# Kernel tuning notes

Hardware: AMD Instinct MI355X
Metric: run time of the kernel (lower is better)

## Reference

```python
import jax, jax.numpy as jnp
import numpy as np

N = 50000      # nodes
E = 800000     # edges (before self loops)
F_IN = 16      # n_input_features
PRE = 32       # n_channels_preproc
C = 128        # n_channels
GH = 32        # edge_gate_hidden_dim
L = 5          # n_gnn_layers (tied weights)


def setup_inputs() -> dict:
    key = jax.random.key(0)
    ks = jax.random.split(key, 16)
    def w(k, shape):
        return jax.random.normal(k, shape, jnp.float32) * 0.05
    return dict(
        x=jax.random.normal(ks[0], (N, F_IN), jnp.float32),
        edge_index=jax.random.randint(ks[1], (2, E), 0, N),
        edge_attr=jax.random.normal(ks[2], (E, 1), jnp.float32),
        W_pre=w(ks[3], (F_IN, PRE)), b_pre=jnp.zeros((PRE,), jnp.float32),
        W_init=w(ks[4], (PRE, C)), b_init=jnp.zeros((C,), jnp.float32),
        W_g1=w(ks[5], (2 * C + 1, GH)), b_g1=jnp.zeros((GH,), jnp.float32),
        W_g2=w(ks[6], (GH, 1)), b_g2=jnp.zeros((1,), jnp.float32),
        W_z=w(ks[7], (2 * C, C)), b_z=jnp.zeros((C,), jnp.float32),
        W_r=w(ks[8], (2 * C, C)), b_r=jnp.zeros((C,), jnp.float32),
        W_h=w(ks[9], (2 * C, C)), b_h=jnp.zeros((C,), jnp.float32),
        W_f1=w(ks[10], (2 * C, C)), b_f1=jnp.zeros((C,), jnp.float32),
        W_f2=w(ks[11], (C, 2)), b_f2=jnp.zeros((2,), jnp.float32),
    )


def reference(x, edge_index, edge_attr,
              W_pre, b_pre, W_init, b_init,
              W_g1, b_g1, W_g2, b_g2,
              W_z, b_z, W_r, b_r, W_h, b_h,
              W_f1, b_f1, W_f2, b_f2):
    n = x.shape[0]
    # add self loops (fill_value=0.0 for edge_attr)
    sl = jnp.arange(n)
    row = jnp.concatenate([edge_index[0], sl])   # source (x_j)
    col = jnp.concatenate([edge_index[1], sl])   # target (x_i), aggregation index
    ea = jnp.concatenate([edge_attr, jnp.zeros((n, 1), x.dtype)], axis=0)
    # symmetric normalization from in-degree (degree of col, incl. self loops)
    deg = jax.ops.segment_sum(jnp.ones(col.shape[0], x.dtype), col, num_segments=n)
    dis = jnp.where(deg > 0, deg ** -0.5, 0.0)
    norm = (dis[row] * dis[col])[:, None]        # [E', 1]

    # preproc + initial node transform
    h = jax.nn.relu(x @ W_pre + b_pre)
    h0 = jax.nn.relu(h @ W_init + b_init)
    h = h0

    for _ in range(L):  # tied GGNN layers
        x_i = h[col]                              # gather target feats  [E', C]
        x_j = h[row]                              # gather source feats  [E', C]
        g_in = jnp.concatenate([x_i, x_j, ea], axis=-1)          # [E', 2C+1]
        gate = jax.nn.sigmoid(jax.nn.relu(g_in @ W_g1 + b_g1) @ W_g2 + b_g2)
        msg = gate * (norm * x_j)                                  # [E', C]
        aggr = jax.ops.segment_sum(msg, col, num_segments=n)       # scatter-add
        # GRU-style update
        za = jnp.concatenate([h, aggr], axis=-1)                   # [N, 2C]
        z = jax.nn.sigmoid(za @ W_z + b_z)
        r = jax.nn.sigmoid(za @ W_r + b_r)
        hc = jax.nn.relu(jnp.concatenate([r * h, aggr], axis=-1) @ W_h + b_h)
        h = (1.0 - z) * h + z * hc

    out = jnp.concatenate([h0, h], axis=-1)       # [N, 2C]
    out = jax.nn.relu(out @ W_f1 + b_f1)
    return out @ W_f2 + b_f2                      # [N, 2] logits (output_activation='none')
```

## Files before the change

kernel.cpp:

```cpp
#include <hip/hip_runtime.h>
#include <math.h>

#define NODES 50000
#define NEDGES 800000
#define ETOT (NEDGES + NODES)
#define FIN 16
#define PRE 32
#define C 128
#define GH 32
#define LAYERS 5
#define RECS 160
#define SCB 64
#define SCT 256
#define SCCH ((NODES + SCB*SCT - 1) / (SCB*SCT))
#define NB ((NODES + 255) >> 8)
#define BCAP 6144
#define LOUTC (BCAP + 256)
#define BIN_BLOCKS 98
#define EPB ((NEDGES + BIN_BLOCKS - 1) / BIN_BLOCKS)

typedef _Float16 f16;
typedef f16 f16x8 __attribute__((ext_vector_type(8)));
typedef f16 f16x4 __attribute__((ext_vector_type(4)));
typedef f16 f16x2 __attribute__((ext_vector_type(2)));
typedef float f32x4 __attribute__((ext_vector_type(4)));

__device__ __forceinline__ float sigmoidf_(float x) { return 1.0f / (1.0f + __expf(-x)); }

__device__ __forceinline__ int swz_off(int row, int bytecol, int stride) {
    return row * stride + ((((bytecol) >> 4) ^ (row & 7)) << 4) + (bytecol & 15);
}
__device__ __forceinline__ int ps_off(int row, int bytecol) {
    return row * 64 + ((((bytecol) >> 4) ^ (row & 3)) << 4) + (bytecol & 15);
}

__device__ __forceinline__ int bperm(int c) { return 4 * (c & 7) + (c >> 3); }

__global__ void k_degree(const int* __restrict__ col, float* __restrict__ deg) {
    int e = blockIdx.x * blockDim.x + threadIdx.x;
    if (e < NEDGES) atomicAdd(&deg[col[e]], 1.0f);
}

__global__ __launch_bounds__(SCT) void k_scan1(const float* __restrict__ deg, int* __restrict__ bsum) {
    __shared__ int ws4[SCT / 64];
    int b = blockIdx.x, t = threadIdx.x;
    int lane = t & 63, wv = t >> 6;
    int base = (b * SCT + t) * SCCH;
    int sum = 0;
#pragma unroll
    for (int j = 0; j < SCCH; j++) {
        int i = base + j;
        if (i < NODES) sum += (int)deg[i] + 1;
    }
#pragma unroll
    for (int off = 32; off > 0; off >>= 1) sum += __shfl_xor(sum, off, 64);
    if (lane == 0) ws4[wv] = sum;
    __syncthreads();
    if (t == 0) {
        int tot = 0;
#pragma unroll
        for (int j = 0; j < SCT / 64; j++) tot += ws4[j];
        bsum[b] = tot;
    }
}

__global__ __launch_bounds__(64) void k_scan2(const int* __restrict__ bsum, int* __restrict__ bscan,
                                              int* __restrict__ start) {
    int t = threadIdx.x;
    int v = (t < SCB) ? bsum[t] : 0;
    int x = v;
#pragma unroll
    for (int off = 1; off < 64; off <<= 1) {
        int tt = __shfl_up(x, off, 64);
        if (t >= off) x += tt;
    }
    if (t < SCB) bscan[t] = x - v;
    if (t == SCB - 1) start[NODES] = x;
}

__global__ __launch_bounds__(SCT) void k_scan3(
    float* __restrict__ deg_dis, float* __restrict__ rdis, const int* __restrict__ bscan,
    int* __restrict__ start) {
    __shared__ int woff[SCT / 64];
    int b = blockIdx.x, t = threadIdx.x;
    int lane = t & 63, wv = t >> 6;
    int base = (b * SCT + t) * SCCH;
    int v[SCCH]; int sum = 0;
#pragma unroll
    for (int j = 0; j < SCCH; j++) {
        int i = base + j;
        v[j] = (i < NODES) ? (int)deg_dis[i] + 1 : 0;
        sum += v[j];
    }
    int x = sum;
#pragma unroll
    for (int off = 1; off < 64; off <<= 1) {
        int tt = __shfl_up(x, off, 64);
        if (lane >= off) x += tt;
    }
    int texcl = x - sum;
    if (lane == 63) woff[wv] = x;
    __syncthreads();
    int wbase = 0;
    for (int j = 0; j < wv; j++) wbase += woff[j];
    int run = bscan[b] + wbase + texcl;
#pragma unroll
    for (int j = 0; j < SCCH; j++) {
        int i = base + j;
        if (i < NODES) {
            start[i] = run;
            float fv = (float)v[j];
            deg_dis[i] = rsqrtf(fv);
            rdis[i] = sqrtf(fv);
        }
        run += v[j];
    }
}

__global__ __launch_bounds__(256) void k_bucket2(
    const int* __restrict__ eidx, const float* __restrict__ eattr,
    int* __restrict__ bcnt , int2* __restrict__ bbuf) {
    __shared__ int cnt[NB];
    __shared__ int gbase[NB];
    __shared__ int cur[NB];
    int b = blockIdx.x, t = threadIdx.x;
    int e0 = b * EPB;
    int e1 = e0 + EPB; if (e1 > NEDGES) e1 = NEDGES;
    for (int i = t; i < NB; i += 256) cnt[i] = 0;
    __syncthreads();
    for (int e = e0 + t; e < e1; e += 256) {
        int ci = eidx[NEDGES + e];
        atomicAdd(&cnt[ci >> 8], 1);
    }
    __syncthreads();
    for (int i = t; i < NB; i += 256) {
        gbase[i] = (cnt[i] > 0) ? atomicAdd(&bcnt[i * 16], cnt[i]) : 0;
        cur[i] = 0;
    }
    __syncthreads();
    for (int e = e0 + t; e < e1; e += 256) {
        int r = eidx[e], ci = eidx[NEDGES + e];
        float ea = eattr[e];
        int bk = ci >> 8;
        int pos = gbase[bk] + atomicAdd(&cur[bk], 1);
        if (pos < BCAP)
            bbuf[(size_t)bk * BCAP + pos] =
                make_int2((r & 0xFFFF) | ((ci & 255) << 16), __float_as_int(ea));
    }
}

__global__ __launch_bounds__(256) void k_csr2(
    const int* __restrict__ bcnt, const int2* __restrict__ bbuf,
    const int* __restrict__ start, int2* __restrict__ esort) {
    __shared__ int2 lout[LOUTC];
    __shared__ int lcur[256];
    int b = blockIdx.x, t = threadIdx.x;
    int lo = b << 8;
    int hi = lo + 256; if (hi > NODES) hi = NODES;
    int nn = hi - lo;
    int sbase = start[lo];
    int total = start[hi] - sbase;
    if (t < nn) lcur[t] = start[lo + t] - sbase;
    __syncthreads();
    int n = bcnt[b * 16]; if (n > BCAP) n = BCAP;
    for (int i = t; i < n; i += 256) {
        int2 w = bbuf[(size_t)b * BCAP + i];
        int cil = (w.x >> 16) & 255;
        int r = w.x & 0xFFFF;
        int pos = atomicAdd(&lcur[cil], 1);
        if (pos < LOUTC) lout[pos] = make_int2(r, w.y);
    }
    if (t < nn) {
        int pos = atomicAdd(&lcur[t], 1);
        if (pos < LOUTC) lout[pos] = make_int2(lo + t, 0);
    }
    __syncthreads();
    int lim = total < LOUTC ? total : LOUTC;
    for (int i = t; i < lim; i += 256) esort[sbase + i] = lout[i];
}

__global__ __launch_bounds__(256) void k_prep_w(
    const float* __restrict__ Wz, const float* __restrict__ Wr, const float* __restrict__ Wh,
    const float* __restrict__ Wg1, const float* __restrict__ Wf1,
    const float* __restrict__ Wpre, const float* __restrict__ Winit,
    f16* __restrict__ WcatF, f16* __restrict__ WhtopF, f16* __restrict__ Wg1F,
    f16* __restrict__ Wf1F, f16* __restrict__ WpreF, f16* __restrict__ WinitF) {
    int t = blockIdx.x * 256 + threadIdx.x;
    int l = t & 63;
    int lr = l & 15, lh = l >> 4;
    if (t < 24 * 8 * 64) {
        int idx = t >> 6; int nt = idx >> 3, ks = idx & 7;
        int wv = nt / 6, ntl = nt % 6;
        int grp = ntl >> 1, pr = ntl & 1;
        int ncol = (2 * wv + pr) * 16 + lr;
        f16x8 v;
#pragma unroll
        for (int j = 0; j < 8; j++) {
            int k = ks * 32 + lh * 8 + j;
            float x;
            if (grp == 0)      x = Wz[k * 128 + ncol];
            else if (grp == 1) x = Wr[k * 128 + ncol];
            else               x = (k >= 128) ? Wh[k * 128 + ncol] : 0.0f;
            v[j] = (f16)x;
        }
        *(f16x8*)(WcatF + (size_t)t * 8) = v;
    } else if (t < 24 * 8 * 64 + 8 * 4 * 64) {
        int t2 = t - 24 * 8 * 64;
        int idx = t2 >> 6; int nt = idx >> 2, ks = idx & 3;
        int n = nt * 16 + lr;
        f16x8 v;
#pragma unroll
        for (int j = 0; j < 8; j++) {
            int k = ks * 32 + lh * 8 + j;
            v[j] = (f16)Wh[k * 128 + n];
        }
        *(f16x8*)(WhtopF + (size_t)t2 * 8) = v;
    } else if (t < 24 * 8 * 64 + 8 * 4 * 64 + 4 * 4 * 64) {
        int t3 = t - (24 * 8 * 64 + 8 * 4 * 64);
        int idx = t3 >> 6; int nt = idx >> 2, ks = idx & 3;
        int cg = nt * 16 + lr;
        f16x8 v;
#pragma unroll
        for (int j = 0; j < 8; j++) {
            int k = ks * 32 + lh * 8 + j;
            v[j] = (f16)((cg < 32) ? Wg1[k * GH + cg] : Wg1[(128 + k) * GH + (cg - 32)]);
        }
        *(f16x8*)(Wg1F + (size_t)t3 * 8) = v;
    } else if (t < 24 * 8 * 64 + 8 * 4 * 64 + 4 * 4 * 64 + 8 * 8 * 64) {
        int t4 = t - (24 * 8 * 64 + 8 * 4 * 64 + 4 * 4 * 64);
        int idx = t4 >> 6; int nt = idx >> 3, ks = idx & 7;
        int n = nt * 16 + lr;
        f16x8 v;
#pragma unroll
        for (int j = 0; j < 8; j++) {
            int k = ks * 32 + lh * 8 + j;
            v[j] = (f16)Wf1[k * 128 + n];
        }
        *(f16x8*)(Wf1F + (size_t)t4 * 8) = v;
    } else if (t < 19456 + 2 * 64) {
        int t5 = t - 19456;
        int nt = t5 >> 6;
        f16x8 v;
#pragma unroll
        for (int j = 0; j < 8; j++) {
            int k = lh * 8 + j;
            v[j] = (k < FIN) ? (f16)Wpre[k * PRE + nt * 16 + lr] : (f16)0.0f;
        }
        *(f16x8*)(WpreF + (size_t)t5 * 8) = v;
    } else if (t < 19456 + 128 + 8 * 64) {
        int t6 = t - 19456 - 128;
        int nt = t6 >> 6;
        f16x8 v;
#pragma unroll
        for (int j = 0; j < 8; j++) {
            int k = lh * 8 + j;
            v[j] = (f16)Winit[k * C + nt * 16 + lr];
        }
        *(f16x8*)(WinitF + (size_t)t6 * 8) = v;
    }
}

__global__ __launch_bounds__(256) void k_pre_gate(
    const float* __restrict__ x, const float* __restrict__ bpre, const float* __restrict__ binit,
    const float* __restrict__ dis,
    const f16* __restrict__ WpreF, const f16* __restrict__ WinitF,
    const f16* __restrict__ Wg1F, const float* __restrict__ bg1,
    f16* __restrict__ h0_16, f16* __restrict__ rec,
    float* __restrict__ A) {
    __shared__ f16 ps[32 * 32];
    __shared__ f16 za[32 * 128];
    char* psB = (char*)ps;
    char* zaB = (char*)za;
    int tid = threadIdx.x;
    int l = tid & 63, w = tid >> 6;
    int lr = l & 15, lh = l >> 4;
    int n0 = blockIdx.x * 32;
    int rt0 = w >> 1, ct = w & 1;

    f16x8 xa = {};
    {
        int gn = n0 + rt0 * 16 + lr;
        if (gn < NODES && lh < 2) {
            float4 xv0 = *(const float4*)(x + (size_t)gn * FIN + lh * 8);
            float4 xv1 = *(const float4*)(x + (size_t)gn * FIN + lh * 8 + 4);
            xa[0] = (f16)xv0.x; xa[1] = (f16)xv0.y; xa[2] = (f16)xv0.z; xa[3] = (f16)xv0.w;
            xa[4] = (f16)xv1.x; xa[5] = (f16)xv1.y; xa[6] = (f16)xv1.z; xa[7] = (f16)xv1.w;
        }
    }
    f16x8 bA = *(const f16x8*)(WpreF + ((size_t)ct * 64 + l) * 8);
    f32x4 accA; accA[0] = accA[1] = accA[2] = accA[3] = 0.0f;
    accA = __builtin_amdgcn_mfma_f32_16x16x32_f16(xa, bA, accA, 0, 0, 0);
    {
        float bp = bpre[ct * 16 + lr];
#pragma unroll
        for (int j = 0; j < 4; j++) {
            int row = rt0 * 16 + lh * 4 + j;
            float v = fmaxf(accA[j] + bp, 0.0f);
            *(f16*)(psB + ps_off(row, (ct * 16 + lr) * 2)) = (f16)v;
        }
    }
    __syncthreads();

    f16x8 pa0 = *(const f16x8*)(psB + ps_off(lr, lh * 16));
    f16x8 pa1 = *(const f16x8*)(psB + ps_off(lr + 16, lh * 16));
    f32x4 accB[2][2];
#pragma unroll
    for (int rt = 0; rt < 2; rt++)
#pragma unroll
        for (int ntl = 0; ntl < 2; ntl++)
#pragma unroll
            for (int j = 0; j < 4; j++) accB[rt][ntl][j] = 0.0f;
#pragma unroll
    for (int ntl = 0; ntl < 2; ntl++) {
        f16x8 b = *(const f16x8*)(WinitF + ((size_t)((w * 2 + ntl) * 64 + l)) * 8);
        accB[0][ntl] = __builtin_amdgcn_mfma_f32_16x16x32_f16(pa0, b, accB[0][ntl], 0, 0, 0);
        accB[1][ntl] = __builtin_amdgcn_mfma_f32_16x16x32_f16(pa1, b, accB[1][ntl], 0, 0, 0);
    }
#pragma unroll
    for (int rt = 0; rt < 2; rt++)
#pragma unroll
        for (int ntl = 0; ntl < 2; ntl++) {
            int cg = (w * 2 + ntl) * 16 + lr;
            float bi = binit[cg];
#pragma unroll
            for (int j = 0; j < 4; j++) {
                int row = rt * 16 + lh * 4 + j;
                float v = fmaxf(accB[rt][ntl][j] + bi, 0.0f);
                *(f16*)(zaB + swz_off(row, cg * 2, 256)) = (f16)v;
            }
        }
    __syncthreads();

    for (int p = tid; p < 32 * 16; p += 256) {
        int row = p >> 4, seg = p & 15;
        int gn = n0 + row;
        if (gn < NODES) {
            f16x8 v = *(const f16x8*)(zaB + swz_off(row, seg * 16, 256));
            *(f16x8*)(h0_16 + (size_t)gn * C + seg * 8) = v;
            float dn = dis[gn];
            f16x8 od;
#pragma unroll
            for (int j = 0; j < 8; j++) od[j] = (f16)((float)v[j] * dn);
            *(f16x8*)(rec + (size_t)gn * RECS + 32 + seg * 8) = od;
        }
    }

    f32x4 acc3[2];
#pragma unroll
    for (int rt = 0; rt < 2; rt++)
#pragma unroll
        for (int j = 0; j < 4; j++) acc3[rt][j] = 0.0f;
#pragma unroll
    for (int ks = 0; ks < 4; ks++) {
        int kk = ks * 32 + lh * 8;
        f16x8 a0 = *(const f16x8*)(zaB + swz_off(lr,      kk * 2, 256));
        f16x8 a1 = *(const f16x8*)(zaB + swz_off(lr + 16, kk * 2, 256));
        f16x8 b = *(const f16x8*)(Wg1F + ((size_t)(w * 4 + ks) * 64 + l) * 8);
        acc3[0] = __builtin_amdgcn_mfma_f32_16x16x32_f16(a0, b, acc3[0], 0, 0, 0);
        acc3[1] = __builtin_amdgcn_mfma_f32_16x16x32_f16(a1, b, acc3[1], 0, 0, 0);
    }
    int col3 = w * 16 + lr;
#pragma unroll
    for (int rt = 0; rt < 2; rt++)
#pragma unroll
        for (int j = 0; j < 4; j++) {
            int row = rt * 16 + lh * 4 + j;
            int gn = n0 + row;
            if (gn < NODES) {
                float v = acc3[rt][j];
                if (col3 < 32) A[(size_t)gn * GH + bperm(col3)] = v + bg1[col3];
                else           rec[(size_t)gn * RECS + bperm(col3 - 32)] = (f16)v;
            }
        }
}

__global__ __launch_bounds__(256) void k_msg(
    const int* __restrict__ start, const int2* __restrict__ esort,
    const float* __restrict__ dis,
    const float* __restrict__ A, const f16* __restrict__ rec,
    const float* __restrict__ Wg1, const float* __restrict__ Wg2, const float* __restrict__ bg2,
    f16* __restrict__ aggr16) {
    int wid = (blockIdx.x * blockDim.x + threadIdx.x) >> 6;
    int lane = threadIdx.x & 63;
    if (wid >= NODES) return;
    int k8 = lane & 7;
    int q = lane >> 3;
    int s0 = start[wid], s1 = start[wid + 1];
    float4 a4 = *(const float4*)(A + (size_t)wid * GH + k8 * 4);
    const float* wg1e = Wg1 + 2 * C * GH;
    float wea0 = wg1e[k8], wea1 = wg1e[k8 + 8], wea2 = wg1e[k8 + 16], wea3 = wg1e[k8 + 24];
    float w20 = Wg2[k8], w21 = Wg2[k8 + 8], w22 = Wg2[k8 + 16], w23 = Wg2[k8 + 24];
    float b2 = bg2[0];
    float dci = dis[wid];
    float acc[16];
#pragma unroll
    for (int j = 0; j < 16; j++) acc[j] = 0.0f;

    int s = s0 + q;
    f16x8 ha0 = {}, hb0 = {};
    f16x4 bb0 = {};
    float ea0 = 0.0f;
    if (s < s1) {
        int2 e0 = esort[s];
        ea0 = __int_as_float(e0.y);
        const f16* rr = rec + (size_t)e0.x * RECS;
        bb0 = *(const f16x4*)(rr + k8 * 4);
        ha0 = *(const f16x8*)(rr + 32 + k8 * 16);
        hb0 = *(const f16x8*)(rr + 32 + k8 * 16 + 8);
    }
    while (s < s1) {
        int s2 = s + 8;
        f16x8 ha1 = {}, hb1 = {};
        f16x4 bb1 = {};
        float ea1 = 0.0f;
        if (s2 < s1) {
            int2 e1 = esort[s2];
            ea1 = __int_as_float(e1.y);
            const f16* rr = rec + (size_t)e1.x * RECS;
            bb1 = *(const f16x4*)(rr + k8 * 4);
            ha1 = *(const f16x8*)(rr + 32 + k8 * 16);
            hb1 = *(const f16x8*)(rr + 32 + k8 * 16 + 8);
        }
        float t0 = fmaxf(a4.x + (float)bb0[0] + ea0 * wea0, 0.0f);
        float t1 = fmaxf(a4.y + (float)bb0[1] + ea0 * wea1, 0.0f);
        float t2 = fmaxf(a4.z + (float)bb0[2] + ea0 * wea2, 0.0f);
        float t3 = fmaxf(a4.w + (float)bb0[3] + ea0 * wea3, 0.0f);
        float p = t0 * w20;
        p = fmaf(t1, w21, p);
        p = fmaf(t2, w22, p);
        p = fmaf(t3, w23, p);
        p += __shfl_xor(p, 4, 8);
        p += __shfl_xor(p, 2, 8);
        p += __shfl_xor(p, 1, 8);
        float coef = sigmoidf_(p + b2);
#pragma unroll
        for (int j = 0; j < 8; j++) {
            acc[j]     = fmaf(coef, (float)ha0[j], acc[j]);
            acc[8 + j] = fmaf(coef, (float)hb0[j], acc[8 + j]);
        }
        ha0 = ha1; hb0 = hb1; bb0 = bb1; ea0 = ea1;
        s = s2;
    }
#pragma unroll
    for (int j = 0; j < 16; j++) {
        acc[j] += __shfl_xor(acc[j], 8, 64);
        acc[j] += __shfl_xor(acc[j], 16, 64);
        acc[j] += __shfl_xor(acc[j], 32, 64);
    }
    if (lane < 8) {
        f16x8 o1, o2;
#pragma unroll
        for (int j = 0; j < 8; j++) { o1[j] = (f16)(acc[j] * dci); o2[j] = (f16)(acc[8 + j] * dci); }
        *(f16x8*)(aggr16 + (size_t)wid * C + k8 * 16) = o1;
        *(f16x8*)(aggr16 + (size_t)wid * C + k8 * 16 + 8) = o2;
    }
}

__global__ __launch_bounds__(256) void k_update_mfma(
    f16* __restrict__ rec, const f16* __restrict__ aggr16,
    const float* __restrict__ dis, const float* __restrict__ rdis,
    const f16* __restrict__ WcatF, const f16* __restrict__ WhtopF, const f16* __restrict__ Wg1F,
    const float* __restrict__ bz, const float* __restrict__ br, const float* __restrict__ bh,
    const float* __restrict__ bg1,
    float* __restrict__ A) {
    __shared__ f16 za[32 * 256];
    __shared__ f16 rhbuf[32 * 128];
    char* zaB = (char*)za;
    char* rhB = (char*)rhbuf;
    int tid = threadIdx.x;
    int l = tid & 63, w = tid >> 6;
    int lr = l & 15, lh = l >> 4;
    int n0 = blockIdx.x * 32;

    for (int p = tid; p < 32 * 16; p += 256) {
        int row = p >> 4, seg = p & 15;
        int gn = n0 + row;
        f16x8 v = {};
        if (gn < NODES) {
            v = *(const f16x8*)(rec + (size_t)gn * RECS + 32 + seg * 8);
            float rd = rdis[gn];
#pragma unroll
            for (int j = 0; j < 8; j++) v[j] = (f16)((float)v[j] * rd);
        }
        *(f16x8*)(zaB + swz_off(row, seg * 16, 512)) = v;
    }
    for (int p = tid; p < 32 * 16; p += 256) {
        int row = p >> 4, seg = p & 15;
        int gn = n0 + row;
        f16x8 v = {};
        if (gn < NODES) v = *(const f16x8*)(aggr16 + (size_t)gn * C + seg * 8);
        *(f16x8*)(zaB + swz_off(row, 256 + seg * 16, 512)) = v;
    }
    __syncthreads();

    f32x4 acc[2][6];
#pragma unroll
    for (int rt = 0; rt < 2; rt++)
#pragma unroll
        for (int n = 0; n < 6; n++)
#pragma unroll
            for (int j = 0; j < 4; j++) acc[rt][n][j] = 0.0f;
#pragma unroll
    for (int ks = 0; ks < 8; ks++) {
        int kk = ks * 32 + lh * 8;
        f16x8 a0 = *(const f16x8*)(zaB + swz_off(lr,      kk * 2, 512));
        f16x8 a1 = *(const f16x8*)(zaB + swz_off(lr + 16, kk * 2, 512));
#pragma unroll
        for (int ntl = 0; ntl < 6; ntl++) {
            f16x8 b = *(const f16x8*)(WcatF + ((size_t)((w * 6 + ntl) * 8 + ks) * 64 + l) * 8);
            acc[0][ntl] = __builtin_amdgcn_mfma_f32_16x16x32_f16(a0, b, acc[0][ntl], 0, 0, 0);
            acc[1][ntl] = __builtin_amdgcn_mfma_f32_16x16x32_f16(a1, b, acc[1][ntl], 0, 0, 0);
        }
    }

    float zreg[2][2][4];
#pragma unroll
    for (int rt = 0; rt < 2; rt++)
#pragma unroll
        for (int pr = 0; pr < 2; pr++) {
            int cg = (2 * w + pr) * 16 + lr;
#pragma unroll
            for (int j = 0; j < 4; j++) {
                int row = rt * 16 + lh * 4 + j;
                zreg[rt][pr][j] = sigmoidf_(acc[rt][pr][j] + bz[cg]);
                float rv = sigmoidf_(acc[rt][2 + pr][j] + br[cg]);
                float hv = (float)*(const f16*)(zaB + swz_off(row, cg * 2, 512));
                *(f16*)(rhB + swz_off(row, cg * 2, 256)) = (f16)(rv * hv);
            }
        }
    __syncthreads();

    f32x4 acc2[2][2];
#pragma unroll
    for (int rt = 0; rt < 2; rt++)
#pragma unroll
        for (int pr = 0; pr < 2; pr++) {
            int cg = (2 * w + pr) * 16 + lr;
#pragma unroll
            for (int j = 0; j < 4; j++)
                acc2[rt][pr][j] = acc[rt][4 + pr][j] + bh[cg];
        }
#pragma unroll
    for (int ks = 0; ks < 4; ks++) {
        int kk = ks * 32 + lh * 8;
        f16x8 a0 = *(const f16x8*)(rhB + swz_off(lr,      kk * 2, 256));
        f16x8 a1 = *(const f16x8*)(rhB + swz_off(lr + 16, kk * 2, 256));
#pragma unroll
        for (int pr = 0; pr < 2; pr++) {
            f16x8 b = *(const f16x8*)(WhtopF + ((size_t)((w * 2 + pr) * 4 + ks) * 64 + l) * 8);
            acc2[0][pr] = __builtin_amdgcn_mfma_f32_16x16x32_f16(a0, b, acc2[0][pr], 0, 0, 0);
            acc2[1][pr] = __builtin_amdgcn_mfma_f32_16x16x32_f16(a1, b, acc2[1][pr], 0, 0, 0);
        }
    }

#pragma unroll
    for (int rt = 0; rt < 2; rt++)
#pragma unroll
        for (int pr = 0; pr < 2; pr++) {
            int cg = (2 * w + pr) * 16 + lr;
#pragma unroll
            for (int j = 0; j < 4; j++) {
                int row = rt * 16 + lh * 4 + j;
                int gn = n0 + row;
                float hc = fmaxf(acc2[rt][pr][j], 0.0f);
                float z = zreg[rt][pr][j];
                float hold = (float)*(const f16*)(zaB + swz_off(row, cg * 2, 512));
                float hn = (1.0f - z) * hold + z * hc;
                if (gn < NODES) {
                    rec[(size_t)gn * RECS + 32 + cg] = (f16)(hn * dis[gn]);
                }
                *(f16*)(zaB + swz_off(row, cg * 2, 512)) = (f16)hn;
            }
        }
    __syncthreads();

    f32x4 acc3[2];
#pragma unroll
    for (int rt = 0; rt < 2; rt++)
#pragma unroll
        for (int j = 0; j < 4; j++) acc3[rt][j] = 0.0f;
#pragma unroll
    for (int ks = 0; ks < 4; ks++) {
        int kk = ks * 32 + lh * 8;
        f16x8 a0 = *(const f16x8*)(zaB + swz_off(lr,      kk * 2, 512));
        f16x8 a1 = *(const f16x8*)(zaB + swz_off(lr + 16, kk * 2, 512));
        f16x8 b = *(const f16x8*)(Wg1F + ((size_t)(w * 4 + ks) * 64 + l) * 8);
        acc3[0] = __builtin_amdgcn_mfma_f32_16x16x32_f16(a0, b, acc3[0], 0, 0, 0);
        acc3[1] = __builtin_amdgcn_mfma_f32_16x16x32_f16(a1, b, acc3[1], 0, 0, 0);
    }
    int col3 = w * 16 + lr;
#pragma unroll
    for (int rt = 0; rt < 2; rt++)
#pragma unroll
        for (int j = 0; j < 4; j++) {
            int row = rt * 16 + lh * 4 + j;
            int gn = n0 + row;
            if (gn < NODES) {
                float v = acc3[rt][j];
                if (col3 < 32) A[(size_t)gn * GH + bperm(col3)] = v + bg1[col3];
                else           rec[(size_t)gn * RECS + bperm(col3 - 32)] = (f16)v;
            }
        }
}

__global__ __launch_bounds__(256) void k_final_mfma(
    const f16* __restrict__ h0_16, const f16* __restrict__ rec, const float* __restrict__ rdis,
    const f16* __restrict__ Wf1F, const float* __restrict__ bf1,
    const float* __restrict__ Wf2, const float* __restrict__ bf2,
    float* __restrict__ out) {
    __shared__ float fs[32][132];
    char* zaB = (char*)&fs[0][0];
    int tid = threadIdx.x;
    int l = tid & 63, w = tid >> 6;
    int lr = l & 15, lh = l >> 4;
    int n0 = blockIdx.x * 32;

    for (int p = tid; p < 32 * 16; p += 256) {
        int row = p >> 4, seg = p & 15;
        int gn = n0 + row;
        f16x8 v = {};
        if (gn < NODES) v = *(const f16x8*)(h0_16 + (size_t)gn * C + seg * 8);
        *(f16x8*)(zaB + swz_off(row, seg * 16, 512)) = v;
    }
    for (int p = tid; p < 32 * 16; p += 256) {
        int row = p >> 4, seg = p & 15;
        int gn = n0 + row;
        f16x8 v = {};
        if (gn < NODES) {
            v = *(const f16x8*)(rec + (size_t)gn * RECS + 32 + seg * 8);
            float rd = rdis[gn];
#pragma unroll
            for (int j = 0; j < 8; j++) v[j] = (f16)((float)v[j] * rd);
        }
        *(f16x8*)(zaB + swz_off(row, 256 + seg * 16, 512)) = v;
    }
    __syncthreads();

    f32x4 acc[2][2];
#pragma unroll
    for (int rt = 0; rt < 2; rt++)
#pragma unroll
        for (int n = 0; n < 2; n++)
#pragma unroll
            for (int j = 0; j < 4; j++) acc[rt][n][j] = 0.0f;
#pragma unroll
    for (int ks = 0; ks < 8; ks++) {
        int kk = ks * 32 + lh * 8;
        f16x8 a0 = *(const f16x8*)(zaB + swz_off(lr,      kk * 2, 512));
        f16x8 a1 = *(const f16x8*)(zaB + swz_off(lr + 16, kk * 2, 512));
#pragma unroll
        for (int ntl = 0; ntl < 2; ntl++) {
            f16x8 b = *(const f16x8*)(Wf1F + ((size_t)((w * 2 + ntl) * 8 + ks) * 64 + l) * 8);
            acc[0][ntl] = __builtin_amdgcn_mfma_f32_16x16x32_f16(a0, b, acc[0][ntl], 0, 0, 0);
            acc[1][ntl] = __builtin_amdgcn_mfma_f32_16x16x32_f16(a1, b, acc[1][ntl], 0, 0, 0);
        }
    }
    __syncthreads();

#pragma unroll
    for (int rt = 0; rt < 2; rt++)
#pragma unroll
        for (int ntl = 0; ntl < 2; ntl++) {
            int cg = (w * 2 + ntl) * 16 + lr;
#pragma unroll
            for (int j = 0; j < 4; j++) {
                int row = rt * 16 + lh * 4 + j;
                fs[row][cg] = fmaxf(acc[rt][ntl][j] + bf1[cg], 0.0f);
            }
        }
    __syncthreads();

    if (tid < 64) {
        int n = tid >> 1, o = tid & 1;
        int gn = n0 + n;
        if (gn < NODES) {
            float a = bf2[o];
#pragma unroll 16
            for (int c = 0; c < C; c++) a = fmaf(fs[n][c], Wf2[c * 2 + o], a);
            out[(size_t)gn * 2 + o] = a;
        }
    }
}

extern "C" void kernel_launch(void* const* d_in, const int* in_sizes, int n_in,
                              void* d_out, int out_size, void* d_ws, size_t ws_size,
                              hipStream_t stream) {
    const float* x    = (const float*)d_in[0];
    const int*   eidx = (const int*)d_in[1];
    const float* eattr= (const float*)d_in[2];
    const float* Wpre = (const float*)d_in[3];  const float* bpre = (const float*)d_in[4];
    const float* Winit= (const float*)d_in[5];  const float* binit= (const float*)d_in[6];
    const float* Wg1  = (const float*)d_in[7];  const float* bg1  = (const float*)d_in[8];
    const float* Wg2  = (const float*)d_in[9];  const float* bg2  = (const float*)d_in[10];
    const float* Wz   = (const float*)d_in[11]; const float* bz   = (const float*)d_in[12];
    const float* Wr   = (const float*)d_in[13]; const float* br   = (const float*)d_in[14];
    const float* Wh   = (const float*)d_in[15]; const float* bh   = (const float*)d_in[16];
    const float* Wf1  = (const float*)d_in[17]; const float* bf1  = (const float*)d_in[18];
    const float* Wf2  = (const float*)d_in[19]; const float* bf2  = (const float*)d_in[20];
    float* out = (float*)d_out;

    float* ws  = (float*)d_ws;
    float* dis = ws;
    float* rdis= dis + NODES;
    float* A   = rdis + NODES;
    int*   start = (int*)(A + (size_t)NODES * GH);
    int*   bsum  = start + NODES + 1;
    int*   bscan = bsum + SCB;
    int*   bcnt  = bscan + SCB;
    int2*  bbuf  = (int2*)(((size_t)(bcnt + NB * 16) + 7) & ~(size_t)7);
    int2*  esort = bbuf + (size_t)NB * BCAP;
    size_t f16_base = (size_t)((int*)(esort + ETOT) - (int*)ws);
    f16_base = (f16_base + 3) & ~(size_t)3;
    f16* h0_16  = (f16*)(ws + f16_base);
    f16* rec    = h0_16 + (size_t)NODES * C;
    f16* aggr16 = rec + (size_t)NODES * RECS;
    f16* WcatF  = aggr16 + (size_t)NODES * C;
    f16* WhtopF = WcatF + 24 * 8 * 64 * 8;
    f16* Wg1F   = WhtopF + 8 * 4 * 64 * 8;
    f16* Wf1F   = Wg1F + 4 * 4 * 64 * 8;
    f16* WpreF  = Wf1F + 8 * 8 * 64 * 8;
    f16* WinitF = WpreF + 2 * 64 * 8;
    size_t f16_total = (size_t)NODES * (C + RECS + C)
                     + (24 * 8 + 8 * 4 + 4 * 4 + 8 * 8 + 2 + 8) * 64 * 8;
    const size_t REQ = (f16_base + (f16_total + 1) / 2) * sizeof(float);
    if (ws_size < REQ) return;

    hipMemsetAsync(dis, 0, NODES * sizeof(float), stream);
    hipMemsetAsync(bcnt, 0, NB * 16 * sizeof(int), stream);
    k_degree<<<(NEDGES + 255) / 256, 256, 0, stream>>>(eidx + NEDGES, dis);
    k_scan1<<<SCB, SCT, 0, stream>>>(dis, bsum);
    k_scan2<<<1, 64, 0, stream>>>(bsum, bscan, start);
    k_scan3<<<SCB, SCT, 0, stream>>>(dis, rdis, bscan, start);
    k_bucket2<<<BIN_BLOCKS, 256, 0, stream>>>(eidx, eattr, bcnt, bbuf);
    k_csr2<<<NB, 256, 0, stream>>>(bcnt, bbuf, start, esort);
    k_prep_w<<<(19456 + 128 + 512 + 255) / 256, 256, 0, stream>>>(
        Wz, Wr, Wh, Wg1, Wf1, Wpre, Winit, WcatF, WhtopF, Wg1F, Wf1F, WpreF, WinitF);
    k_pre_gate<<<(NODES + 31) / 32, 256, 0, stream>>>(
        x, bpre, binit, dis, WpreF, WinitF, Wg1F, bg1, h0_16, rec, A);

    for (int l = 0; l < LAYERS; l++) {
        k_msg<<<(NODES * 64 + 255) / 256, 256, 0, stream>>>(
            start, esort, dis, A, rec, Wg1, Wg2, bg2, aggr16);
        k_update_mfma<<<(NODES + 31) / 32, 256, 0, stream>>>(
            rec, aggr16, dis, rdis, WcatF, WhtopF, Wg1F, bz, br, bh, bg1, A);
    }
    k_final_mfma<<<(NODES + 31) / 32, 256, 0, stream>>>(h0_16, rec, rdis, Wf1F, bf1, Wf2, bf2, out);
}
```

Baseline: 557.8 us.

## Fuse message aggregation into GRU update kernel with ping-pong node buffers

Merges the per-node gated message aggregation kernel into the MFMA update kernel, so each block aggregates its 32 nodes directly into shared memory instead of writing and re-reading an f16 aggregate array. To avoid read/write races on node records across blocks, the record and gate-precompute arrays are double-buffered and swapped each layer. This removes one launch per layer and the aggr round trip. In exchange, each block of 256 threads now serialises 8 nodes per wave in the gather phase and may have lower occupancy, because the aggregation phase and the MFMA phase now live in one kernel that uses the shared-memory tiles.

```diff
diff --git a/kernel.cpp b/kernel.cpp
--- a/kernel.cpp
+++ b/kernel.cpp
@@ -374,95 +374,15 @@
         }
 }
 
-__global__ __launch_bounds__(256) void k_msg(
+__global__ __launch_bounds__(256) void k_layer(
     const int* __restrict__ start, const int2* __restrict__ esort,
-    const float* __restrict__ dis,
-    const float* __restrict__ A, const f16* __restrict__ rec,
+    const float* __restrict__ dis, const float* __restrict__ rdis,
+    const float* __restrict__ A_cur, const f16* __restrict__ recC,
+    f16* __restrict__ recN, float* __restrict__ A_nxt,
+    const f16* __restrict__ WcatF, const f16* __restrict__ WhtopF, const f16* __restrict__ Wg1F,
     const float* __restrict__ Wg1, const float* __restrict__ Wg2, const float* __restrict__ bg2,
-    f16* __restrict__ aggr16) {
-    int wid = (blockIdx.x * blockDim.x + threadIdx.x) >> 6;
-    int lane = threadIdx.x & 63;
-    if (wid >= NODES) return;
-    int k8 = lane & 7;
-    int q = lane >> 3;
-    int s0 = start[wid], s1 = start[wid + 1];
-    float4 a4 = *(const float4*)(A + (size_t)wid * GH + k8 * 4);
-    const float* wg1e = Wg1 + 2 * C * GH;
-    float wea0 = wg1e[k8], wea1 = wg1e[k8 + 8], wea2 = wg1e[k8 + 16], wea3 = wg1e[k8 + 24];
-    float w20 = Wg2[k8], w21 = Wg2[k8 + 8], w22 = Wg2[k8 + 16], w23 = Wg2[k8 + 24];
-    float b2 = bg2[0];
-    float dci = dis[wid];
-    float acc[16];
-#pragma unroll
-    for (int j = 0; j < 16; j++) acc[j] = 0.0f;
-
-    int s = s0 + q;
-    f16x8 ha0 = {}, hb0 = {};
-    f16x4 bb0 = {};
-    float ea0 = 0.0f;
-    if (s < s1) {
-        int2 e0 = esort[s];
-        ea0 = __int_as_float(e0.y);
-        const f16* rr = rec + (size_t)e0.x * RECS;
-        bb0 = *(const f16x4*)(rr + k8 * 4);
-        ha0 = *(const f16x8*)(rr + 32 + k8 * 16);
-        hb0 = *(const f16x8*)(rr + 32 + k8 * 16 + 8);
-    }
-    while (s < s1) {
-        int s2 = s + 8;
-        f16x8 ha1 = {}, hb1 = {};
-        f16x4 bb1 = {};
-        float ea1 = 0.0f;
-        if (s2 < s1) {
-            int2 e1 = esort[s2];
-            ea1 = __int_as_float(e1.y);
-            const f16* rr = rec + (size_t)e1.x * RECS;
-            bb1 = *(const f16x4*)(rr + k8 * 4);
-            ha1 = *(const f16x8*)(rr + 32 + k8 * 16);
-            hb1 = *(const f16x8*)(rr + 32 + k8 * 16 + 8);
-        }
-        float t0 = fmaxf(a4.x + (float)bb0[0] + ea0 * wea0, 0.0f);
-        float t1 = fmaxf(a4.y + (float)bb0[1] + ea0 * wea1, 0.0f);
-        float t2 = fmaxf(a4.z + (float)bb0[2] + ea0 * wea2, 0.0f);
-        float t3 = fmaxf(a4.w + (float)bb0[3] + ea0 * wea3, 0.0f);
-        float p = t0 * w20;
-        p = fmaf(t1, w21, p);
-        p = fmaf(t2, w22, p);
-        p = fmaf(t3, w23, p);
-        p += __shfl_xor(p, 4, 8);
-        p += __shfl_xor(p, 2, 8);
-        p += __shfl_xor(p, 1, 8);
-        float coef = sigmoidf_(p + b2);
-#pragma unroll
-        for (int j = 0; j < 8; j++) {
-            acc[j]     = fmaf(coef, (float)ha0[j], acc[j]);
-            acc[8 + j] = fmaf(coef, (float)hb0[j], acc[8 + j]);
-        }
-        ha0 = ha1; hb0 = hb1; bb0 = bb1; ea0 = ea1;
-        s = s2;
-    }
-#pragma unroll
-    for (int j = 0; j < 16; j++) {
-        acc[j] += __shfl_xor(acc[j], 8, 64);
-        acc[j] += __shfl_xor(acc[j], 16, 64);
-        acc[j] += __shfl_xor(acc[j], 32, 64);
-    }
-    if (lane < 8) {
-        f16x8 o1, o2;
-#pragma unroll
-        for (int j = 0; j < 8; j++) { o1[j] = (f16)(acc[j] * dci); o2[j] = (f16)(acc[8 + j] * dci); }
-        *(f16x8*)(aggr16 + (size_t)wid * C + k8 * 16) = o1;
-        *(f16x8*)(aggr16 + (size_t)wid * C + k8 * 16 + 8) = o2;
-    }
-}
-
-__global__ __launch_bounds__(256) void k_update_mfma(
-    f16* __restrict__ rec, const f16* __restrict__ aggr16,
-    const float* __restrict__ dis, const float* __restrict__ rdis,
-    const f16* __restrict__ WcatF, const f16* __restrict__ WhtopF, const f16* __restrict__ Wg1F,
     const float* __restrict__ bz, const float* __restrict__ br, const float* __restrict__ bh,
-    const float* __restrict__ bg1,
-    float* __restrict__ A) {
+    const float* __restrict__ bg1) {
     __shared__ f16 za[32 * 256];
     __shared__ f16 rhbuf[32 * 128];
     char* zaB = (char*)za;
@@ -477,19 +397,97 @@
         int gn = n0 + row;
         f16x8 v = {};
         if (gn < NODES) {
-            v = *(const f16x8*)(rec + (size_t)gn * RECS + 32 + seg * 8);
+            v = *(const f16x8*)(recC + (size_t)gn * RECS + 32 + seg * 8);
             float rd = rdis[gn];
 #pragma unroll
             for (int j = 0; j < 8; j++) v[j] = (f16)((float)v[j] * rd);
         }
         *(f16x8*)(zaB + swz_off(row, seg * 16, 512)) = v;
     }
-    for (int p = tid; p < 32 * 16; p += 256) {
-        int row = p >> 4, seg = p & 15;
-        int gn = n0 + row;
-        f16x8 v = {};
-        if (gn < NODES) v = *(const f16x8*)(aggr16 + (size_t)gn * C + seg * 8);
-        *(f16x8*)(zaB + swz_off(row, 256 + seg * 16, 512)) = v;
+
+    {
+        int k8 = l & 7;
+        int q = l >> 3;
+        const float* wg1e = Wg1 + 2 * C * GH;
+        float wea0 = wg1e[k8], wea1 = wg1e[k8 + 8], wea2 = wg1e[k8 + 16], wea3 = wg1e[k8 + 24];
+        float w20 = Wg2[k8], w21 = Wg2[k8 + 8], w22 = Wg2[k8 + 16], w23 = Wg2[k8 + 24];
+        float b2 = bg2[0];
+        for (int i = 0; i < 8; i++) {
+            int row = w * 8 + i;
+            int gn = n0 + row;
+            int s0 = 0, s1 = 0;
+            float dci = 0.0f;
+            float4 a4 = make_float4(0.0f, 0.0f, 0.0f, 0.0f);
+            if (gn < NODES) {
+                s0 = start[gn]; s1 = start[gn + 1];
+                dci = dis[gn];
+                a4 = *(const float4*)(A_cur + (size_t)gn * GH + k8 * 4);
+            }
+            float acc[16];
+#pragma unroll
+            for (int j = 0; j < 16; j++) acc[j] = 0.0f;
+            int s = s0 + q;
+            f16x8 ha0 = {}, hb0 = {};
+            f16x4 bb0 = {};
+            float ea0 = 0.0f;
+            if (s < s1) {
+                int2 e0 = esort[s];
+                ea0 = __int_as_float(e0.y);
+                const f16* rr = recC + (size_t)e0.x * RECS;
+                bb0 = *(const f16x4*)(rr + k8 * 4);
+                ha0 = *(const f16x8*)(rr + 32 + k8 * 16);
+                hb0 = *(const f16x8*)(rr + 32 + k8 * 16 + 8);
+            }
+            while (s < s1) {
+                int s2 = s + 8;
+                f16x8 ha1 = {}, hb1 = {};
+                f16x4 bb1 = {};
+                float ea1 = 0.0f;
+                if (s2 < s1) {
+                    int2 e1 = esort[s2];
+                    ea1 = __int_as_float(e1.y);
+                    const f16* rr = recC + (size_t)e1.x * RECS;
+                    bb1 = *(const f16x4*)(rr + k8 * 4);
+                    ha1 = *(const f16x8*)(rr + 32 + k8 * 16);
+                    hb1 = *(const f16x8*)(rr + 32 + k8 * 16 + 8);
+                }
+                float t0 = fmaxf(a4.x + (float)bb0[0] + ea0 * wea0, 0.0f);
+                float t1 = fmaxf(a4.y + (float)bb0[1] + ea0 * wea1, 0.0f);
+                float t2 = fmaxf(a4.z + (float)bb0[2] + ea0 * wea2, 0.0f);
+                float t3 = fmaxf(a4.w + (float)bb0[3] + ea0 * wea3, 0.0f);
+                float p = t0 * w20;
+                p = fmaf(t1, w21, p);
+                p = fmaf(t2, w22, p);
+                p = fmaf(t3, w23, p);
+                p += __shfl_xor(p, 4, 8);
+                p += __shfl_xor(p, 2, 8);
+                p += __shfl_xor(p, 1, 8);
+                float coef = sigmoidf_(p + b2);
+#pragma unroll
+                for (int j = 0; j < 8; j++) {
+                    acc[j]     = fmaf(coef, (float)ha0[j], acc[j]);
+                    acc[8 + j] = fmaf(coef, (float)hb0[j], acc[8 + j]);
+                }
+                ha0 = ha1; hb0 = hb1; bb0 = bb1; ea0 = ea1;
+                s = s2;
+            }
+#pragma unroll
+            for (int j = 0; j < 16; j++) {
+                acc[j] += __shfl_xor(acc[j], 8, 64);
+                acc[j] += __shfl_xor(acc[j], 16, 64);
+                acc[j] += __shfl_xor(acc[j], 32, 64);
+            }
+            if (l < 8) {
+                f16x8 o1, o2;
+#pragma unroll
+                for (int j = 0; j < 8; j++) {
+                    o1[j] = (f16)(acc[j] * dci);
+                    o2[j] = (f16)(acc[8 + j] * dci);
+                }
+                *(f16x8*)(zaB + swz_off(row, 256 + k8 * 32, 512)) = o1;
+                *(f16x8*)(zaB + swz_off(row, 256 + k8 * 32 + 16, 512)) = o2;
+            }
+        }
     }
     __syncthreads();
 
@@ -567,7 +565,7 @@
                 float hold = (float)*(const f16*)(zaB + swz_off(row, cg * 2, 512));
                 float hn = (1.0f - z) * hold + z * hc;
                 if (gn < NODES) {
-                    rec[(size_t)gn * RECS + 32 + cg] = (f16)(hn * dis[gn]);
+                    recN[(size_t)gn * RECS + 32 + cg] = (f16)(hn * dis[gn]);
                 }
                 *(f16*)(zaB + swz_off(row, cg * 2, 512)) = (f16)hn;
             }
@@ -597,8 +595,8 @@
             int gn = n0 + row;
             if (gn < NODES) {
                 float v = acc3[rt][j];
-                if (col3 < 32) A[(size_t)gn * GH + bperm(col3)] = v + bg1[col3];
-                else           rec[(size_t)gn * RECS + bperm(col3 - 32)] = (f16)v;
+                if (col3 < 32) A_nxt[(size_t)gn * GH + bperm(col3)] = v + bg1[col3];
+                else           recN[(size_t)gn * RECS + bperm(col3 - 32)] = (f16)v;
             }
         }
 }
@@ -702,8 +700,9 @@
     float* ws  = (float*)d_ws;
     float* dis = ws;
     float* rdis= dis + NODES;
-    float* A   = rdis + NODES;
-    int*   start = (int*)(A + (size_t)NODES * GH);
+    float* A0  = rdis + NODES;
+    float* A1  = A0 + (size_t)NODES * GH;
+    int*   start = (int*)(A1 + (size_t)NODES * GH);
     int*   bsum  = start + NODES + 1;
     int*   bscan = bsum + SCB;
     int*   bcnt  = bscan + SCB;
@@ -712,15 +711,15 @@
     size_t f16_base = (size_t)((int*)(esort + ETOT) - (int*)ws);
     f16_base = (f16_base + 3) & ~(size_t)3;
     f16* h0_16  = (f16*)(ws + f16_base);
-    f16* rec    = h0_16 + (size_t)NODES * C;
-    f16* aggr16 = rec + (size_t)NODES * RECS;
-    f16* WcatF  = aggr16 + (size_t)NODES * C;
+    f16* rec0   = h0_16 + (size_t)NODES * C;
+    f16* rec1   = rec0 + (size_t)NODES * RECS;
+    f16* WcatF  = rec1 + (size_t)NODES * RECS;
     f16* WhtopF = WcatF + 24 * 8 * 64 * 8;
     f16* Wg1F   = WhtopF + 8 * 4 * 64 * 8;
     f16* Wf1F   = Wg1F + 4 * 4 * 64 * 8;
     f16* WpreF  = Wf1F + 8 * 8 * 64 * 8;
     f16* WinitF = WpreF + 2 * 64 * 8;
-    size_t f16_total = (size_t)NODES * (C + RECS + C)
+    size_t f16_total = (size_t)NODES * (C + 2 * RECS)
                      + (24 * 8 + 8 * 4 + 4 * 4 + 8 * 8 + 2 + 8) * 64 * 8;
     const size_t REQ = (f16_base + (f16_total + 1) / 2) * sizeof(float);
     if (ws_size < REQ) return;
@@ -736,13 +735,17 @@
     k_prep_w<<<(19456 + 128 + 512 + 255) / 256, 256, 0, stream>>>(
         Wz, Wr, Wh, Wg1, Wf1, Wpre, Winit, WcatF, WhtopF, Wg1F, Wf1F, WpreF, WinitF);
     k_pre_gate<<<(NODES + 31) / 32, 256, 0, stream>>>(
-        x, bpre, binit, dis, WpreF, WinitF, Wg1F, bg1, h0_16, rec, A);
+        x, bpre, binit, dis, WpreF, WinitF, Wg1F, bg1, h0_16, rec0, A0);
 
     for (int l = 0; l < LAYERS; l++) {
-        k_msg<<<(NODES * 64 + 255) / 256, 256, 0, stream>>>(
-            start, esort, dis, A, rec, Wg1, Wg2, bg2, aggr16);
-        k_update_mfma<<<(NODES + 31) / 32, 256, 0, stream>>>(
-            rec, aggr16, dis, rdis, WcatF, WhtopF, Wg1F, bz, br, bh, bg1, A);
-    }
-    k_final_mfma<<<(NODES + 31) / 32, 256, 0, stream>>>(h0_16, rec, rdis, Wf1F, bf1, Wf2, bf2, out);
-}
+        f16* recC = (l & 1) ? rec1 : rec0;
+        f16* recN = (l & 1) ? rec0 : rec1;
+        float* Ac = (l & 1) ? A1 : A0;
+        float* An = (l & 1) ? A0 : A1;
+        k_layer<<<(NODES + 31) / 32, 256, 0, stream>>>(
+            start, esort, dis, rdis, Ac, recC, recN, An,
+            WcatF, WhtopF, Wg1F, Wg1, Wg2, bg2, bz, br, bh, bg1);
+    }
+    k_final_mfma<<<(NODES + 31) / 32, 256, 0, stream>>>(
+        h0_16, rec1, rdis, Wf1F, bf1, Wf2, bf2, out);
+}
```

Result: slower. 791.0 us (+41.8%).
